# Optimization experiments

Hardware: AMD Instinct MI355X
Metric: run time of the kernel (lower is better)

The kernel has to match this reference:

```python
import jax, jax.numpy as jnp
import numpy as np

B, N, IN_DIM, OUT_DIM, E = 2, 100000, 128, 128, 600000


def setup_inputs() -> dict:
    key = jax.random.key(0)
    ks = jax.random.split(key, 16)
    inp = {
        'x': jax.random.normal(ks[0], (B, N, IN_DIM), dtype=jnp.float32),
        'edges_r0': jax.random.randint(ks[1], (2, E), 0, N, dtype=jnp.int64),
        'edges_r1': jax.random.randint(ks[2], (2, E), 0, N, dtype=jnp.int64),
        'edges_r2': jax.random.randint(ks[3], (2, E), 0, N, dtype=jnp.int64),
    }
    s = 1.0 / np.sqrt(IN_DIM)
    for i in range(3):
        inp[f'w{i}'] = jax.random.uniform(ks[4 + 3 * i], (OUT_DIM, IN_DIM), minval=-s, maxval=s, dtype=jnp.float32)
        inp[f'gw{i}'] = jax.random.uniform(ks[5 + 3 * i], (2 * OUT_DIM, IN_DIM), minval=-s, maxval=s, dtype=jnp.float32)
        inp[f'gb{i}'] = jax.random.uniform(ks[6 + 3 * i], (2 * OUT_DIM,), minval=-s, maxval=s, dtype=jnp.float32)
    return inp


def _film_conv(x, edges_list, w_list, gw_list, gb_list):
    # x: (B,N,F). For each relation: gather src/dst, linear, FiLM, scatter_add on dst.
    Bn, Nn, _ = x.shape
    out = jnp.zeros((Bn, Nn, OUT_DIM), dtype=x.dtype)
    for edge_index, w, gw, gb in zip(edges_list, w_list, gw_list, gb_list):
        src, dst = edge_index[0], edge_index[1]
        x_src = x[:, src, :]                       # (B,E,F)
        msg_lin = jnp.einsum('bef,of->beo', x_src, w)
        x_dst = x[:, dst, :]                       # (B,E,F)
        film = jnp.einsum('bef,of->beo', x_dst, gw) + gb
        omega, mu = film[..., :OUT_DIM], film[..., OUT_DIM:]
        msg = jax.nn.relu(jax.nn.sigmoid(omega) * msg_lin + mu)
        out = out.at[:, dst, :].add(msg)
    return out


def reference(x, edges_r0, edges_r1, edges_r2, w0, w1, w2, gw0, gb0, gw1, gb1, gw2, gb2):
    return _film_conv(x, [edges_r0, edges_r1, edges_r2], [w0, w1, w2],
                      [gw0, gw1, gw2], [gb0, gb1, gb2])
```

## Files before the change

kernel.cpp:

```cpp
#include <hip/hip_runtime.h>

#define Bn 2
#define Nn 100000
#define DIM 128
#define En 600000
#define MTOT (Bn * Nn)

typedef __attribute__((ext_vector_type(8))) short bf16x8;
typedef __attribute__((ext_vector_type(4))) float f32x4;

__device__ __forceinline__ unsigned short f2bf(float f) {
    union { float f; unsigned u; } v; v.f = f;
    unsigned r = v.u + 0x7fffu + ((v.u >> 16) & 1u);
    return (unsigned short)(r >> 16);
}
__device__ __forceinline__ float bf2f(unsigned u16) {
    union { unsigned u; float f; } v; v.u = u16 << 16; return v.f;
}
__device__ __forceinline__ float bf_lo(unsigned u) {
    union { unsigned u; float f; } v; v.u = u << 16; return v.f;
}
__device__ __forceinline__ float bf_hi(unsigned u) {
    union { unsigned u; float f; } v; v.u = u & 0xffff0000u; return v.f;
}

__global__ __launch_bounds__(256) void cvt_x_kernel(const float4* __restrict__ x,
                                                    ushort4* __restrict__ xbf) {
    int i = blockIdx.x * 256 + threadIdx.x;
    float4 v = x[i];
    ushort4 o;
    o.x = f2bf(v.x); o.y = f2bf(v.y); o.z = f2bf(v.z); o.w = f2bf(v.w);
    xbf[i] = o;
}

__global__ __launch_bounds__(256) void cvt_w_kernel(
    const float* __restrict__ w0,  const float* __restrict__ gw0,
    const float* __restrict__ w1,  const float* __restrict__ gw1,
    const float* __restrict__ w2,  const float* __restrict__ gw2,
    unsigned short* __restrict__ WB)
{
    int idx = blockIdx.x * 256 + threadIdx.x;
    int r = idx / 49152;
    int j = idx - r * 49152;
    const float* w  = (r == 0) ? w0  : (r == 1 ? w1  : w2);
    const float* gw = (r == 0) ? gw0 : (r == 1 ? gw1 : gw2);
    float v = (j < 128 * 128) ? w[j] : gw[j - 128 * 128];
    WB[idx] = f2bf(v);
}

__global__ __launch_bounds__(256) void count_kernel(
    const int* __restrict__ e0, const int* __restrict__ e1, const int* __restrict__ e2,
    int* __restrict__ counts)
{
    int idx = blockIdx.x * 256 + threadIdx.x;
    if (idx >= 3 * En) return;
    int r = (idx >= 2 * En) ? 2 : (idx >= En ? 1 : 0);
    int e = idx - r * En;
    const int* ed = (r == 0) ? e0 : (r == 1 ? e1 : e2);
    int dst = ed[En + e];
    atomicAdd(&counts[r * Nn + dst], 1);
}

#define WPR 1563
__global__ __launch_bounds__(256) void alloc_kernel(
    const int* __restrict__ counts,
    int* __restrict__ starts,
    int* __restrict__ gcursor)
{
    int wid  = blockIdx.x * 4 + (threadIdx.x >> 6);
    int lane = threadIdx.x & 63;
    int r = wid / WPR;
    if (r >= 3) return;
    int dst = (wid - r * WPR) * 64 + lane;
    int c = (dst < Nn) ? counts[r * Nn + dst] : 0;

    int inc = c;
#pragma unroll
    for (int d = 1; d < 64; d <<= 1) {
        int v = __shfl_up(inc, d);
        if (lane >= d) inc += v;
    }
    int total = __shfl(inc, 63);
    int base = 0;
    if (lane == 63) base = atomicAdd(&gcursor[r], total);
    base = __shfl(base, 63);

    if (dst < Nn) starts[r * Nn + dst] = base + inc - c;
}

__global__ __launch_bounds__(256) void fill_kernel(
    const int* __restrict__ e0, const int* __restrict__ e1, const int* __restrict__ e2,
    const int* __restrict__ starts,
    int* __restrict__ cursor,
    int* __restrict__ records)
{
    int idx = blockIdx.x * 256 + threadIdx.x;
    if (idx >= 3 * En) return;
    int r = (idx >= 2 * En) ? 2 : (idx >= En ? 1 : 0);
    int e = idx - r * En;
    const int* ed = (r == 0) ? e0 : (r == 1 ? e1 : e2);
    int src = ed[e];
    int dst = ed[En + e];
    int pos = atomicAdd(&cursor[r * Nn + dst], 1);
    records[(size_t)r * En + starts[r * Nn + dst] + pos] = src;
}

__global__ __launch_bounds__(256) void transform_kernel(
    const short* __restrict__ Xbf,
    const short* __restrict__ WB,
    const float* __restrict__ gb,
    unsigned short* __restrict__ Abuf,
    unsigned short* __restrict__ Sbuf,
    unsigned short* __restrict__ Mbuf)
{
    __shared__ unsigned short tile[64 * 384];
    const int tid  = threadIdx.x;
    const int wave = tid >> 6;
    const int lane = tid & 63;
    const int m = lane & 15;
    const int q = lane >> 4;
    const size_t nbase = (size_t)blockIdx.x * 64;

    bf16x8 a[4][4];
#pragma unroll
    for (int sub = 0; sub < 4; ++sub)
#pragma unroll
        for (int c = 0; c < 4; ++c)
            a[sub][c] = *(const bf16x8*)(Xbf + (nbase + (size_t)(sub * 16 + m)) * DIM + c * 32 + q * 8);

#pragma unroll
    for (int t = 0; t < 6; ++t) {
        const int ob = wave * 96 + t * 16;
        bf16x8 bfr[4];
#pragma unroll
        for (int c = 0; c < 4; ++c)
            bfr[c] = *(const bf16x8*)(WB + (size_t)(ob + m) * DIM + c * 32 + q * 8);

        f32x4 acc[4];
#pragma unroll
        for (int sub = 0; sub < 4; ++sub) {
            acc[sub] = (f32x4){0.f, 0.f, 0.f, 0.f};
#pragma unroll
            for (int c = 0; c < 4; ++c)
                acc[sub] = __builtin_amdgcn_mfma_f32_16x16x32_bf16(bfr[c], a[sub][c], acc[sub], 0, 0, 0);
        }

        const int o0 = ob + q * 4;
        float4 g = make_float4(0.f, 0.f, 0.f, 0.f);
        if (ob >= 128) g = *(const float4*)(gb + (o0 - 128));

#pragma unroll
        for (int sub = 0; sub < 4; ++sub) {
            const int row = sub * 16 + m;
            float v0 = acc[sub][0], v1 = acc[sub][1], v2 = acc[sub][2], v3 = acc[sub][3];
            if (ob >= 256) {
                v0 += g.x; v1 += g.y; v2 += g.z; v3 += g.w;
            } else if (ob >= 128) {
                v0 = 1.f / (1.f + __expf(-(v0 + g.x)));
                v1 = 1.f / (1.f + __expf(-(v1 + g.y)));
                v2 = 1.f / (1.f + __expf(-(v2 + g.z)));
                v3 = 1.f / (1.f + __expf(-(v3 + g.w)));
            }
            ushort4 o4;
            o4.x = f2bf(v0); o4.y = f2bf(v1); o4.z = f2bf(v2); o4.w = f2bf(v3);
            *(ushort4*)&tile[row * 384 + (o0 ^ ((row & 7) << 3))] = o4;
        }
    }

    __syncthreads();

    const int r16 = tid >> 4;
    const int c8  = (tid & 15) * 8;
#pragma unroll
    for (int it = 0; it < 4; ++it) {
        const int row = it * 16 + r16;
        const int swz = (row & 7) << 3;
        const size_t node = nbase + (size_t)row;
        uint4 va = *(const uint4*)&tile[row * 384 + ((  0 + c8) ^ swz)];
        uint4 vs = *(const uint4*)&tile[row * 384 + ((128 + c8) ^ swz)];
        uint4 vm = *(const uint4*)&tile[row * 384 + ((256 + c8) ^ swz)];
        *(uint4*)(Abuf + node * DIM + c8) = va;
        *(uint4*)(Sbuf + node * DIM + c8) = vs;
        *(uint4*)(Mbuf + node * DIM + c8) = vm;
    }
}

template <int FIRST>
__global__ __launch_bounds__(256) void accum_kernel(
    const unsigned short* __restrict__ Abuf,
    const unsigned short* __restrict__ Sbuf,
    const unsigned short* __restrict__ Mbuf,
    const int* __restrict__ starts,
    const int* __restrict__ counts,
    const int* __restrict__ records,
    float* __restrict__ out)
{
    const int dst  = blockIdx.x * 4 + (threadIdx.x >> 6);
    const int lane = threadIdx.x & 63;
    const int half = lane >> 5;
    const int hl   = lane & 31;
    const int k    = hl * 4;

    const int cnt = counts[dst];
    if (!FIRST && cnt == 0) return;
    const int beg = starts[dst];

    const size_t drow = ((size_t)half * Nn + (size_t)dst) * DIM;

    const uint2 sv = *(const uint2*)(Sbuf + drow + k);
    const uint2 mv = *(const uint2*)(Mbuf + drow + k);
    const float s0 = bf_lo(sv.x), s1 = bf_hi(sv.x), s2 = bf_lo(sv.y), s3 = bf_hi(sv.y);
    const float u0 = bf_lo(mv.x), u1 = bf_hi(mv.x), u2 = bf_lo(mv.y), u3 = bf_hi(mv.y);

    float a0 = 0.f, a1 = 0.f, a2 = 0.f, a3 = 0.f;
    float b0 = 0.f, b1 = 0.f, b2 = 0.f, b3 = 0.f;

    const char* Abase = (const char*)(Abuf + (size_t)half * Nn * DIM + k);

    for (int base = 0; base < cnt; base += 64) {
        const int rem = cnt - base;
        const int nb  = rem < 64 ? rem : 64;
        int srcl = 0;
        if (lane < nb) srcl = records[beg + base + lane];

        int j = 0;
        for (; j + 1 < nb; j += 2) {
            const int sA = __builtin_amdgcn_readlane(srcl, j);
            const int sB = __builtin_amdgcn_readlane(srcl, j + 1);
            const uint2 avA = *(const uint2*)(Abase + (size_t)sA * (DIM * 2));
            const uint2 avB = *(const uint2*)(Abase + (size_t)sB * (DIM * 2));
            float r;
            r = fmaf(s0, bf_lo(avA.x), u0); a0 += fmaxf(r, 0.f);
            r = fmaf(s1, bf_hi(avA.x), u1); a1 += fmaxf(r, 0.f);
            r = fmaf(s2, bf_lo(avA.y), u2); a2 += fmaxf(r, 0.f);
            r = fmaf(s3, bf_hi(avA.y), u3); a3 += fmaxf(r, 0.f);
            r = fmaf(s0, bf_lo(avB.x), u0); b0 += fmaxf(r, 0.f);
            r = fmaf(s1, bf_hi(avB.x), u1); b1 += fmaxf(r, 0.f);
            r = fmaf(s2, bf_lo(avB.y), u2); b2 += fmaxf(r, 0.f);
            r = fmaf(s3, bf_hi(avB.y), u3); b3 += fmaxf(r, 0.f);
        }
        if (j < nb) {
            const int sA = __builtin_amdgcn_readlane(srcl, j);
            const uint2 avA = *(const uint2*)(Abase + (size_t)sA * (DIM * 2));
            float r;
            r = fmaf(s0, bf_lo(avA.x), u0); a0 += fmaxf(r, 0.f);
            r = fmaf(s1, bf_hi(avA.x), u1); a1 += fmaxf(r, 0.f);
            r = fmaf(s2, bf_lo(avA.y), u2); a2 += fmaxf(r, 0.f);
            r = fmaf(s3, bf_hi(avA.y), u3); a3 += fmaxf(r, 0.f);
        }
    }
    a0 += b0; a1 += b1; a2 += b2; a3 += b3;

    float4* op = (float4*)(out + drow + k);
    if (FIRST) {
        *op = make_float4(a0, a1, a2, a3);
    } else {
        float4 v = *op;
        v.x += a0; v.y += a1; v.z += a2; v.w += a3;
        *op = v;
    }
}

__global__ __launch_bounds__(128) void fallback_kernel(
    const float* __restrict__ x,
    const int* __restrict__ edges,
    const float* __restrict__ w,
    const float* __restrict__ gw,
    const float* __restrict__ gb,
    float* __restrict__ out)
{
    __shared__ float xs[DIM], xd[DIM];
    int be = blockIdx.x;
    int e = be >> 1, b = be & 1;
    int t = threadIdx.x;
    int src = edges[e], dst = edges[En + e];
    xs[t] = x[((size_t)b * Nn + src) * DIM + t];
    xd[t] = x[((size_t)b * Nn + dst) * DIM + t];
    __syncthreads();
    float ml = 0.f, om = gb[t], mu = gb[128 + t];
    for (int kk = 0; kk < DIM; ++kk) {
        float xsk = xs[kk], xdk = xd[kk];
        ml += w[t * DIM + kk] * xsk;
        om += gw[t * DIM + kk] * xdk;
        mu += gw[(128 + t) * DIM + kk] * xdk;
    }
    float s = 1.f / (1.f + __expf(-om));
    float msg = s * ml + mu;
    msg = msg > 0.f ? msg : 0.f;
    unsafeAtomicAdd(out + ((size_t)b * Nn + dst) * DIM + t, msg);
}

extern "C" void kernel_launch(void* const* d_in, const int* in_sizes, int n_in,
                              void* d_out, int out_size, void* d_ws, size_t ws_size,
                              hipStream_t stream) {
    const float* x    = (const float*)d_in[0];
    const int*   ed[3] = { (const int*)d_in[1],
                           (const int*)d_in[2],
                           (const int*)d_in[3] };
    const float* w[3]  = { (const float*)d_in[4], (const float*)d_in[7], (const float*)d_in[10] };
    const float* gw[3] = { (const float*)d_in[5], (const float*)d_in[8], (const float*)d_in[11] };
    const float* gb[3] = { (const float*)d_in[6], (const float*)d_in[9], (const float*)d_in[12] };
    float* out = (float*)d_out;

    const size_t xbf_sz  = (size_t)MTOT * DIM * 2;
    const size_t wb_sz   = (size_t)3 * 384 * DIM * 2;
    const size_t buf_sz  = (size_t)MTOT * DIM * 2;
    const size_t cnt_sz  = (size_t)3 * Nn * 4;
    const size_t cur_sz  = (size_t)3 * Nn * 4;
    const size_t gcu_sz  = 64;
    const size_t sta_sz  = (size_t)3 * Nn * 4;
    const size_t rec_sz  = (size_t)3 * En * 4;
    const size_t need    = xbf_sz + wb_sz + 3 * buf_sz + cnt_sz + cur_sz + gcu_sz + sta_sz + rec_sz + 1024;

    if (ws_size >= need) {
        char* p = (char*)d_ws;
        short*          Xbf = (short*)p;              p += xbf_sz;
        unsigned short* WB  = (unsigned short*)p;     p += wb_sz;
        unsigned short* Ab  = (unsigned short*)p;     p += buf_sz;
        unsigned short* Sb  = (unsigned short*)p;     p += buf_sz;
        unsigned short* Mb  = (unsigned short*)p;     p += buf_sz;
        int*            counts  = (int*)p;            p += cnt_sz;
        int*            cursor  = (int*)p;            p += cur_sz;
        int*            gcursor = (int*)p;            p += gcu_sz;
        int*            starts  = (int*)p;            p += sta_sz;
        int*            records = (int*)p;

        hipMemsetAsync(counts, 0, cnt_sz + cur_sz + gcu_sz, stream);

        cvt_x_kernel<<<(MTOT * DIM / 4) / 256, 256, 0, stream>>>((const float4*)x, (ushort4*)Xbf);
        cvt_w_kernel<<<(3 * 384 * DIM) / 256, 256, 0, stream>>>(
            w[0], gw[0], w[1], gw[1], w[2], gw[2], WB);

        count_kernel<<<(3 * En + 255) / 256, 256, 0, stream>>>(ed[0], ed[1], ed[2], counts);
        alloc_kernel<<<(3 * WPR + 3) / 4, 256, 0, stream>>>(counts, starts, gcursor);
        fill_kernel<<<(3 * En + 255) / 256, 256, 0, stream>>>(ed[0], ed[1], ed[2], starts, cursor, records);

        for (int r = 0; r < 3; ++r) {
            transform_kernel<<<MTOT / 64, 256, 0, stream>>>(
                Xbf, (const short*)(WB + (size_t)r * 384 * DIM), gb[r], Ab, Sb, Mb);
            const int* sta = starts + (size_t)r * Nn;
            const int* cnt = counts + (size_t)r * Nn;
            const int* rec = records + (size_t)r * En;
            if (r == 0)
                accum_kernel<1><<<Nn / 4, 256, 0, stream>>>(Ab, Sb, Mb, sta, cnt, rec, out);
            else
                accum_kernel<0><<<Nn / 4, 256, 0, stream>>>(Ab, Sb, Mb, sta, cnt, rec, out);
        }
    } else {
        hipMemsetAsync(d_out, 0, (size_t)MTOT * DIM * sizeof(float), stream);
        for (int r = 0; r < 3; ++r)
            fallback_kernel<<<En * Bn, 128, 0, stream>>>(x, ed[r], w[r], gw[r], gb[r], out);
    }
}
```

Baseline: 910.6 us.

## Fuse FiLM gate/shift GEMM into gather-accumulate kernel, drop S/M buffers

The transform kernel now computes only the source linear projection. The FiLM sigmoid-gate and shift GEMM for destination nodes moves into the accumulation kernel, which computes it for 32 destinations per block into shared memory before gathering. This removes writing and re-reading two full bf16 intermediate buffers per relation. In exchange, each wave serially processes 8 destinations, which reduces parallelism for the latency-bound gather and may worsen load imbalance.

```diff
diff --git a/kernel.cpp b/kernel.cpp
--- a/kernel.cpp
+++ b/kernel.cpp
@@ -5,6 +5,7 @@
 #define DIM 128
 #define En 600000
 #define MTOT (Bn * Nn)
+#define DPB 32
 
 typedef __attribute__((ext_vector_type(8))) short bf16x8;
 typedef __attribute__((ext_vector_type(4))) float f32x4;
@@ -105,15 +106,12 @@
     records[(size_t)r * En + starts[r * Nn + dst] + pos] = src;
 }
 
-__global__ __launch_bounds__(256) void transform_kernel(
+__global__ __launch_bounds__(256) void transformA_kernel(
     const short* __restrict__ Xbf,
     const short* __restrict__ WB,
-    const float* __restrict__ gb,
-    unsigned short* __restrict__ Abuf,
-    unsigned short* __restrict__ Sbuf,
-    unsigned short* __restrict__ Mbuf)
-{
-    __shared__ unsigned short tile[64 * 384];
+    unsigned short* __restrict__ Abuf)
+{
+    __shared__ unsigned short tile[64 * 128];
     const int tid  = threadIdx.x;
     const int wave = tid >> 6;
     const int lane = tid & 63;
@@ -129,41 +127,25 @@
             a[sub][c] = *(const bf16x8*)(Xbf + (nbase + (size_t)(sub * 16 + m)) * DIM + c * 32 + q * 8);
 
 #pragma unroll
-    for (int t = 0; t < 6; ++t) {
-        const int ob = wave * 96 + t * 16;
+    for (int t = 0; t < 2; ++t) {
+        const int ob = wave * 32 + t * 16;
         bf16x8 bfr[4];
 #pragma unroll
         for (int c = 0; c < 4; ++c)
             bfr[c] = *(const bf16x8*)(WB + (size_t)(ob + m) * DIM + c * 32 + q * 8);
 
-        f32x4 acc[4];
+        const int o0 = ob + q * 4;
 #pragma unroll
         for (int sub = 0; sub < 4; ++sub) {
-            acc[sub] = (f32x4){0.f, 0.f, 0.f, 0.f};
+            f32x4 acc = (f32x4){0.f, 0.f, 0.f, 0.f};
 #pragma unroll
             for (int c = 0; c < 4; ++c)
-                acc[sub] = __builtin_amdgcn_mfma_f32_16x16x32_bf16(bfr[c], a[sub][c], acc[sub], 0, 0, 0);
-        }
-
-        const int o0 = ob + q * 4;
-        float4 g = make_float4(0.f, 0.f, 0.f, 0.f);
-        if (ob >= 128) g = *(const float4*)(gb + (o0 - 128));
-
-#pragma unroll
-        for (int sub = 0; sub < 4; ++sub) {
+                acc = __builtin_amdgcn_mfma_f32_16x16x32_bf16(bfr[c], a[sub][c], acc, 0, 0, 0);
             const int row = sub * 16 + m;
-            float v0 = acc[sub][0], v1 = acc[sub][1], v2 = acc[sub][2], v3 = acc[sub][3];
-            if (ob >= 256) {
-                v0 += g.x; v1 += g.y; v2 += g.z; v3 += g.w;
-            } else if (ob >= 128) {
-                v0 = 1.f / (1.f + __expf(-(v0 + g.x)));
-                v1 = 1.f / (1.f + __expf(-(v1 + g.y)));
-                v2 = 1.f / (1.f + __expf(-(v2 + g.z)));
-                v3 = 1.f / (1.f + __expf(-(v3 + g.w)));
-            }
             ushort4 o4;
-            o4.x = f2bf(v0); o4.y = f2bf(v1); o4.z = f2bf(v2); o4.w = f2bf(v3);
-            *(ushort4*)&tile[row * 384 + (o0 ^ ((row & 7) << 3))] = o4;
+            o4.x = f2bf(acc[0]); o4.y = f2bf(acc[1]);
+            o4.z = f2bf(acc[2]); o4.w = f2bf(acc[3]);
+            *(ushort4*)&tile[row * 128 + (o0 ^ ((row & 7) << 3))] = o4;
         }
     }
 
@@ -176,88 +158,143 @@
         const int row = it * 16 + r16;
         const int swz = (row & 7) << 3;
         const size_t node = nbase + (size_t)row;
-        uint4 va = *(const uint4*)&tile[row * 384 + ((  0 + c8) ^ swz)];
-        uint4 vs = *(const uint4*)&tile[row * 384 + ((128 + c8) ^ swz)];
-        uint4 vm = *(const uint4*)&tile[row * 384 + ((256 + c8) ^ swz)];
+        uint4 va = *(const uint4*)&tile[row * 128 + (c8 ^ swz)];
         *(uint4*)(Abuf + node * DIM + c8) = va;
-        *(uint4*)(Sbuf + node * DIM + c8) = vs;
-        *(uint4*)(Mbuf + node * DIM + c8) = vm;
     }
 }
 
 template <int FIRST>
-__global__ __launch_bounds__(256) void accum_kernel(
+__global__ __launch_bounds__(256) void film_accum_kernel(
+    const short* __restrict__ Xbf,
+    const short* __restrict__ GWB,
+    const float* __restrict__ gb,
     const unsigned short* __restrict__ Abuf,
-    const unsigned short* __restrict__ Sbuf,
-    const unsigned short* __restrict__ Mbuf,
     const int* __restrict__ starts,
     const int* __restrict__ counts,
     const int* __restrict__ records,
     float* __restrict__ out)
 {
-    const int dst  = blockIdx.x * 4 + (threadIdx.x >> 6);
-    const int lane = threadIdx.x & 63;
+    __shared__ unsigned short smtile[64 * 256];
+    const int tid  = threadIdx.x;
+    const int wave = tid >> 6;
+    const int lane = tid & 63;
+    const int m = lane & 15;
+    const int q = lane >> 4;
+    const int dbase = blockIdx.x * DPB;
+
+    {
+        bf16x8 a[4][4];
+#pragma unroll
+        for (int rt = 0; rt < 4; ++rt) {
+            const int i = rt * 16 + m;
+            const int b = i >> 5;
+            const int local = i & 31;
+            const size_t grow = (size_t)b * Nn + (size_t)(dbase + local);
+#pragma unroll
+            for (int c = 0; c < 4; ++c)
+                a[rt][c] = *(const bf16x8*)(Xbf + grow * DIM + c * 32 + q * 8);
+        }
+
+        const int obase = wave * 64;
+#pragma unroll
+        for (int t = 0; t < 4; ++t) {
+            const int ot = obase + t * 16;
+            bf16x8 bfr[4];
+#pragma unroll
+            for (int c = 0; c < 4; ++c)
+                bfr[c] = *(const bf16x8*)(GWB + (size_t)(ot + m) * DIM + c * 32 + q * 8);
+
+            const int o0 = ot + q * 4;
+            const float4 g = *(const float4*)(gb + o0);
+#pragma unroll
+            for (int rt = 0; rt < 4; ++rt) {
+                f32x4 acc = (f32x4){0.f, 0.f, 0.f, 0.f};
+#pragma unroll
+                for (int c = 0; c < 4; ++c)
+                    acc = __builtin_amdgcn_mfma_f32_16x16x32_bf16(bfr[c], a[rt][c], acc, 0, 0, 0);
+                float v0 = acc[0] + g.x, v1 = acc[1] + g.y;
+                float v2 = acc[2] + g.z, v3 = acc[3] + g.w;
+                if (obase < 128) {
+                    v0 = 1.f / (1.f + __expf(-v0));
+                    v1 = 1.f / (1.f + __expf(-v1));
+                    v2 = 1.f / (1.f + __expf(-v2));
+                    v3 = 1.f / (1.f + __expf(-v3));
+                }
+                const int xrow = rt * 16 + m;
+                ushort4 o4;
+                o4.x = f2bf(v0); o4.y = f2bf(v1); o4.z = f2bf(v2); o4.w = f2bf(v3);
+                *(ushort4*)&smtile[xrow * 256 + (o0 ^ ((xrow & 7) << 3))] = o4;
+            }
+        }
+    }
+
+    __syncthreads();
+
     const int half = lane >> 5;
     const int hl   = lane & 31;
     const int k    = hl * 4;
-
-    const int cnt = counts[dst];
-    if (!FIRST && cnt == 0) return;
-    const int beg = starts[dst];
-
-    const size_t drow = ((size_t)half * Nn + (size_t)dst) * DIM;
-
-    const uint2 sv = *(const uint2*)(Sbuf + drow + k);
-    const uint2 mv = *(const uint2*)(Mbuf + drow + k);
-    const float s0 = bf_lo(sv.x), s1 = bf_hi(sv.x), s2 = bf_lo(sv.y), s3 = bf_hi(sv.y);
-    const float u0 = bf_lo(mv.x), u1 = bf_hi(mv.x), u2 = bf_lo(mv.y), u3 = bf_hi(mv.y);
-
-    float a0 = 0.f, a1 = 0.f, a2 = 0.f, a3 = 0.f;
-    float b0 = 0.f, b1 = 0.f, b2 = 0.f, b3 = 0.f;
-
     const char* Abase = (const char*)(Abuf + (size_t)half * Nn * DIM + k);
 
-    for (int base = 0; base < cnt; base += 64) {
-        const int rem = cnt - base;
-        const int nb  = rem < 64 ? rem : 64;
-        int srcl = 0;
-        if (lane < nb) srcl = records[beg + base + lane];
-
-        int j = 0;
-        for (; j + 1 < nb; j += 2) {
-            const int sA = __builtin_amdgcn_readlane(srcl, j);
-            const int sB = __builtin_amdgcn_readlane(srcl, j + 1);
-            const uint2 avA = *(const uint2*)(Abase + (size_t)sA * (DIM * 2));
-            const uint2 avB = *(const uint2*)(Abase + (size_t)sB * (DIM * 2));
-            float r;
-            r = fmaf(s0, bf_lo(avA.x), u0); a0 += fmaxf(r, 0.f);
-            r = fmaf(s1, bf_hi(avA.x), u1); a1 += fmaxf(r, 0.f);
-            r = fmaf(s2, bf_lo(avA.y), u2); a2 += fmaxf(r, 0.f);
-            r = fmaf(s3, bf_hi(avA.y), u3); a3 += fmaxf(r, 0.f);
-            r = fmaf(s0, bf_lo(avB.x), u0); b0 += fmaxf(r, 0.f);
-            r = fmaf(s1, bf_hi(avB.x), u1); b1 += fmaxf(r, 0.f);
-            r = fmaf(s2, bf_lo(avB.y), u2); b2 += fmaxf(r, 0.f);
-            r = fmaf(s3, bf_hi(avB.y), u3); b3 += fmaxf(r, 0.f);
-        }
-        if (j < nb) {
-            const int sA = __builtin_amdgcn_readlane(srcl, j);
-            const uint2 avA = *(const uint2*)(Abase + (size_t)sA * (DIM * 2));
-            float r;
-            r = fmaf(s0, bf_lo(avA.x), u0); a0 += fmaxf(r, 0.f);
-            r = fmaf(s1, bf_hi(avA.x), u1); a1 += fmaxf(r, 0.f);
-            r = fmaf(s2, bf_lo(avA.y), u2); a2 += fmaxf(r, 0.f);
-            r = fmaf(s3, bf_hi(avA.y), u3); a3 += fmaxf(r, 0.f);
-        }
-    }
-    a0 += b0; a1 += b1; a2 += b2; a3 += b3;
-
-    float4* op = (float4*)(out + drow + k);
-    if (FIRST) {
-        *op = make_float4(a0, a1, a2, a3);
-    } else {
-        float4 v = *op;
-        v.x += a0; v.y += a1; v.z += a2; v.w += a3;
-        *op = v;
+    for (int ii = 0; ii < 8; ++ii) {
+        const int dl  = wave * 8 + ii;
+        const int dst = dbase + dl;
+        const int cnt = counts[dst];
+        if (!FIRST && cnt == 0) continue;
+        const int beg = starts[dst];
+
+        const int xrow = half * 32 + dl;
+        const int swz  = (xrow & 7) << 3;
+        const ushort4 sv = *(const ushort4*)&smtile[xrow * 256 + (k ^ swz)];
+        const ushort4 mv = *(const ushort4*)&smtile[xrow * 256 + ((128 + k) ^ swz)];
+        const float s0 = bf2f(sv.x), s1 = bf2f(sv.y), s2 = bf2f(sv.z), s3 = bf2f(sv.w);
+        const float u0 = bf2f(mv.x), u1 = bf2f(mv.y), u2 = bf2f(mv.z), u3 = bf2f(mv.w);
+
+        float a0 = 0.f, a1 = 0.f, a2 = 0.f, a3 = 0.f;
+        float b0 = 0.f, b1 = 0.f, b2 = 0.f, b3 = 0.f;
+
+        for (int base = 0; base < cnt; base += 64) {
+            const int rem = cnt - base;
+            const int nb  = rem < 64 ? rem : 64;
+            int srcl = 0;
+            if (lane < nb) srcl = records[beg + base + lane];
+
+            int j = 0;
+            for (; j + 1 < nb; j += 2) {
+                const int sA = __builtin_amdgcn_readlane(srcl, j);
+                const int sB = __builtin_amdgcn_readlane(srcl, j + 1);
+                const uint2 avA = *(const uint2*)(Abase + (size_t)sA * (DIM * 2));
+                const uint2 avB = *(const uint2*)(Abase + (size_t)sB * (DIM * 2));
+                float r;
+                r = fmaf(s0, bf_lo(avA.x), u0); a0 += fmaxf(r, 0.f);
+                r = fmaf(s1, bf_hi(avA.x), u1); a1 += fmaxf(r, 0.f);
+                r = fmaf(s2, bf_lo(avA.y), u2); a2 += fmaxf(r, 0.f);
+                r = fmaf(s3, bf_hi(avA.y), u3); a3 += fmaxf(r, 0.f);
+                r = fmaf(s0, bf_lo(avB.x), u0); b0 += fmaxf(r, 0.f);
+                r = fmaf(s1, bf_hi(avB.x), u1); b1 += fmaxf(r, 0.f);
+                r = fmaf(s2, bf_lo(avB.y), u2); b2 += fmaxf(r, 0.f);
+                r = fmaf(s3, bf_hi(avB.y), u3); b3 += fmaxf(r, 0.f);
+            }
+            if (j < nb) {
+                const int sA = __builtin_amdgcn_readlane(srcl, j);
+                const uint2 avA = *(const uint2*)(Abase + (size_t)sA * (DIM * 2));
+                float r;
+                r = fmaf(s0, bf_lo(avA.x), u0); a0 += fmaxf(r, 0.f);
+                r = fmaf(s1, bf_hi(avA.x), u1); a1 += fmaxf(r, 0.f);
+                r = fmaf(s2, bf_lo(avA.y), u2); a2 += fmaxf(r, 0.f);
+                r = fmaf(s3, bf_hi(avA.y), u3); a3 += fmaxf(r, 0.f);
+            }
+        }
+        a0 += b0; a1 += b1; a2 += b2; a3 += b3;
+
+        const size_t drow = ((size_t)half * Nn + (size_t)dst) * DIM;
+        float4* op = (float4*)(out + drow + k);
+        if (FIRST) {
+            *op = make_float4(a0, a1, a2, a3);
+        } else {
+            float4 v = *op;
+            v.x += a0; v.y += a1; v.z += a2; v.w += a3;
+            *op = v;
+        }
     }
 }
 
@@ -310,15 +347,13 @@
     const size_t gcu_sz  = 64;
     const size_t sta_sz  = (size_t)3 * Nn * 4;
     const size_t rec_sz  = (size_t)3 * En * 4;
-    const size_t need    = xbf_sz + wb_sz + 3 * buf_sz + cnt_sz + cur_sz + gcu_sz + sta_sz + rec_sz + 1024;
+    const size_t need    = xbf_sz + wb_sz + buf_sz + cnt_sz + cur_sz + gcu_sz + sta_sz + rec_sz + 1024;
 
     if (ws_size >= need) {
         char* p = (char*)d_ws;
         short*          Xbf = (short*)p;              p += xbf_sz;
         unsigned short* WB  = (unsigned short*)p;     p += wb_sz;
         unsigned short* Ab  = (unsigned short*)p;     p += buf_sz;
-        unsigned short* Sb  = (unsigned short*)p;     p += buf_sz;
-        unsigned short* Mb  = (unsigned short*)p;     p += buf_sz;
         int*            counts  = (int*)p;            p += cnt_sz;
         int*            cursor  = (int*)p;            p += cur_sz;
         int*            gcursor = (int*)p;            p += gcu_sz;
@@ -336,15 +371,19 @@
         fill_kernel<<<(3 * En + 255) / 256, 256, 0, stream>>>(ed[0], ed[1], ed[2], starts, cursor, records);
 
         for (int r = 0; r < 3; ++r) {
-            transform_kernel<<<MTOT / 64, 256, 0, stream>>>(
-                Xbf, (const short*)(WB + (size_t)r * 384 * DIM), gb[r], Ab, Sb, Mb);
+            const unsigned short* WBr  = WB + (size_t)r * 384 * DIM;
+            const unsigned short* GWBr = WBr + (size_t)128 * DIM;
+            transformA_kernel<<<MTOT / 64, 256, 0, stream>>>(
+                Xbf, (const short*)WBr, Ab);
             const int* sta = starts + (size_t)r * Nn;
             const int* cnt = counts + (size_t)r * Nn;
             const int* rec = records + (size_t)r * En;
             if (r == 0)
-                accum_kernel<1><<<Nn / 4, 256, 0, stream>>>(Ab, Sb, Mb, sta, cnt, rec, out);
+                film_accum_kernel<1><<<Nn / DPB, 256, 0, stream>>>(
+                    Xbf, (const short*)GWBr, gb[r], Ab, sta, cnt, rec, out);
             else
-                accum_kernel<0><<<Nn / 4, 256, 0, stream>>>(Ab, Sb, Mb, sta, cnt, rec, out);
+                film_accum_kernel<0><<<Nn / DPB, 256, 0, stream>>>(
+                    Xbf, (const short*)GWBr, gb[r], Ab, sta, cnt, rec, out);
         }
     } else {
         hipMemsetAsync(d_out, 0, (size_t)MTOT * DIM * sizeof(float), stream);
```

Result: no change. 920.8 us (+1.1%).
